# Kernel optimization log

Hardware: AMD Instinct MI355X
Metric: run time of the kernel (lower is better)

The kernel has to match this reference:

```python
import jax, jax.numpy as jnp
import numpy as np
import math

N_FILT = 80
FILT_DIM = 251
FS = 16000
MIN_FREQ = 50.0
MIN_BAND = 50.0


def _init_params():
    low_freq_mel = 80.0
    high_freq_mel = 2595.0 * np.log10(1.0 + FS / 2.0 / 700.0)
    mel_points = np.linspace(low_freq_mel, high_freq_mel, N_FILT)
    f_cos = 700.0 * (10.0 ** (mel_points / 2595.0) - 1.0)
    b1 = np.roll(f_cos, 1)
    b2 = np.roll(f_cos, -1)
    b1[0] = 30.0
    b2[-1] = FS / 2.0 - 100.0
    freq_scale = FS * 1.0
    return (jnp.asarray(b1 / freq_scale, dtype=jnp.float32),
            jnp.asarray((b2 - b1) / freq_scale, dtype=jnp.float32))


def setup_inputs() -> dict:
    key = jax.random.key(0)
    x = jax.random.normal(key, (32, 1, 32000), dtype=jnp.float32)
    filt_b1, filt_band = _init_params()
    return {"x": x, "filt_b1": filt_b1, "filt_band": filt_band}


def _sinc_batch(band, t_right):
    # band: [F] (in Hz, already scaled by fs); t_right: [T] (seconds)
    arg = 2.0 * math.pi * band[:, None] * t_right[None, :]  # [F, T]
    y_right = jnp.sin(arg) / arg
    y_left = y_right[:, ::-1]
    ones = jnp.ones((band.shape[0], 1), dtype=band.dtype)
    return jnp.concatenate([y_left, ones, y_right], axis=1)  # [F, 2T+1]


def _build_filters(filt_b1, filt_band):
    N = FILT_DIM
    freq_scale = float(FS)
    t_right = (jnp.linspace(1.0, (N - 1) / 2.0, (N - 1) // 2) / FS).astype(jnp.float32)
    filt_beg = jnp.abs(filt_b1) + MIN_FREQ / freq_scale            # [F]
    filt_end = filt_beg + (jnp.abs(filt_band) + MIN_BAND / freq_scale)
    # torch.linspace(0, N, steps=N): N points from 0 to N inclusive
    n = jnp.linspace(0.0, float(N), N).astype(jnp.float32)
    window = (0.54 - 0.46 * jnp.cos(2.0 * math.pi * n / N)).astype(jnp.float32)
    low_pass1 = 2.0 * filt_beg[:, None] * _sinc_batch(filt_beg * freq_scale, t_right)
    low_pass2 = 2.0 * filt_end[:, None] * _sinc_batch(filt_end * freq_scale, t_right)
    band_pass = low_pass2 - low_pass1                              # [F, N]
    band_pass = band_pass / jnp.max(band_pass, axis=1, keepdims=True)
    return band_pass * window[None, :]                             # [F, N]


def reference(x, filt_b1, filt_band):
    filters = _build_filters(filt_b1, filt_band)                   # [N_filt, Filt_dim]
    out = jax.lax.conv_general_dilated(
        x, filters[:, None, :],
        window_strides=(1,), padding='VALID',
        dimension_numbers=('NCH', 'OIH', 'NCH'))
    return out  # [B, N_filt, L - Filt_dim + 1]
```

## Files before the change

### kernel.cpp

```cpp
#include <hip/hip_runtime.h>
#include <math.h>

#define N_FILT   80
#define FILT_DIM 251
#define KPAD     256
#define SIG_LEN  32000
#define OUT_LEN  31750
#define BATCH    32
#define TPB      320

#define STRIP    1024
#define NREP     8
#define LROW     644
#define OBS2     36

#define TWO_PI_F 6.28318530717958647692f

typedef __attribute__((ext_vector_type(8))) short    short8;
typedef __attribute__((ext_vector_type(8))) _Float16 half8;
typedef __attribute__((ext_vector_type(4))) float    float4v;
typedef __attribute__((ext_vector_type(2))) float    float2v;

__global__ __launch_bounds__(256) void build_filters_kernel(
    const float* __restrict__ b1, const float* __restrict__ band,
    unsigned short* __restrict__ fh)
{
    const int f = blockIdx.x;
    const int i = threadIdx.x;

    const float MINF = 50.0f / 16000.0f;
    const float fb = fabsf(b1[f]) + MINF;
    const float fe = fb + fabsf(band[f]) + MINF;

    float v = 0.0f;
    if (i < FILT_DIM) {
        int m = i - 125; m = (m < 0) ? -m : m;
        if (m == 0) v = 2.0f * fe - 2.0f * fb;
        else {
            float a1 = TWO_PI_F * fb * (float)m;
            float a2 = TWO_PI_F * fe * (float)m;
            v = 2.0f * fe * (sinf(a2) / a2) - 2.0f * fb * (sinf(a1) / a1);
        }
    }

    __shared__ float red[256];
    red[i] = (i < FILT_DIM) ? v : -INFINITY;
    __syncthreads();
    #pragma unroll
    for (int s = 128; s > 0; s >>= 1) {
        if (i < s) red[i] = fmaxf(red[i], red[i + s]);
        __syncthreads();
    }
    const float mx = red[0];

    const float w   = 0.54f - 0.46f * cosf(TWO_PI_F * (float)i / 250.0f);
    const float val = (i < FILT_DIM) ? (v / mx) * w : 0.0f;
    const _Float16 h = (_Float16)val;
    fh[f * KPAD + i] = __builtin_bit_cast(unsigned short, h);
}

__global__ __launch_bounds__(TPB, 7) void sinc_mfma_kernel(
    const float* __restrict__ x,
    const unsigned short* __restrict__ fh,
    float* __restrict__ out)
{
    __shared__ __align__(16) unsigned xf[NREP * LROW];
    __shared__ __align__(16) float    ob[5][16 * OBS2];

    const int tid = threadIdx.x;
    const unsigned raw = blockIdx.x;
    const unsigned swz = (raw & 7u) * 128u + (raw >> 3);
    const int strip = (int)(swz & 31u);
    const int n     = (int)(swz >> 5);
    const int e0    = strip * STRIP;
    const float* xp = x + (size_t)n * SIG_LEN;

    for (int d = tid; d < LROW; d += TPB) {
        const int g = e0 + 2 * d;
        float v0, v1, v2;
        if (g + 2 < SIG_LEN) {
            float2 p = *(const float2*)(xp + g);
            v0 = p.x; v1 = p.y; v2 = xp[g + 2];
        } else {
            v0 = (g     < SIG_LEN) ? xp[g]     : 0.0f;
            v1 = (g + 1 < SIG_LEN) ? xp[g + 1] : 0.0f;
            v2 = (g + 2 < SIG_LEN) ? xp[g + 2] : 0.0f;
        }
        const _Float16 h0 = (_Float16)v0, h1 = (_Float16)v1, h2 = (_Float16)v2;
        union { _Float16 h[2]; unsigned u; } pe, po;
        pe.h[0] = h0; pe.h[1] = h1;
        po.h[0] = h1; po.h[1] = h2;
        xf[0 * LROW + d] = pe.u;
        xf[1 * LROW + d] = po.u;
        if (d >= 1) { xf[2 * LROW + d - 1] = pe.u;
                      xf[3 * LROW + d - 1] = po.u; }
        if (d >= 2) { xf[4 * LROW + d - 2] = pe.u;
                      xf[5 * LROW + d - 2] = po.u; }
        if (d >= 3) { xf[6 * LROW + d - 3] = pe.u;
                      xf[7 * LROW + d - 3] = po.u; }
    }

    const int lane = tid & 63;
    const int w    = tid >> 6;
    const int m    = lane & 15;
    const int q    = lane >> 4;
    short8 Ah[8];
    {
        const unsigned short* ph = fh + (w * 16 + m) * KPAD + q * 8;
        #pragma unroll
        for (int kb = 0; kb < 8; ++kb)
            Ah[kb] = *(const short8*)(ph + kb * 32);
    }
    __syncthreads();

    const int r = m & 7;
    const unsigned base = (unsigned)(r * LROW + 4 * (m >> 3) + 4 * q);

    float* const obw  = &ob[w][0];
    const int    cp   = 2 * (lane & 15);
    const int    rr0  = lane >> 4;
    const size_t row0 = ((size_t)n * N_FILT + w * 16) * OUT_LEN;

    for (int gp = 0; gp < 32; ++gp) {
        #pragma unroll
        for (int tl = 0; tl < 2; ++tl) {
            const int tt = gp * 2 + tl;
            float4v a0 = {0.f,0.f,0.f,0.f}, a1 = {0.f,0.f,0.f,0.f};
            const unsigned o0 = base + 8u * (unsigned)tt;
            #pragma unroll
            for (int kk = 0; kk < 4; ++kk) {
                a0 = __builtin_amdgcn_mfma_f32_16x16x32_f16(
                         __builtin_bit_cast(half8, Ah[2*kk]),
                         __builtin_bit_cast(half8, *(const uint4*)(&xf[o0 + 32*kk])),
                         a0, 0, 0, 0);
                a1 = __builtin_amdgcn_mfma_f32_16x16x32_f16(
                         __builtin_bit_cast(half8, Ah[2*kk+1]),
                         __builtin_bit_cast(half8, *(const uint4*)(&xf[o0 + 32*kk + 16])),
                         a1, 0, 0, 0);
            }
            const int oc = tl * 16 + m;
            #pragma unroll
            for (int rg = 0; rg < 4; ++rg)
                obw[(q * 4 + rg) * OBS2 + oc] = a0[rg] + a1[rg];
        }

        const int t0 = e0 + gp * 32 + cp;
        if (t0 + 1 < OUT_LEN) {
            #pragma unroll
            for (int j = 0; j < 4; ++j) {
                const int row = j * 4 + rr0;
                const float2v v = *(const float2v*)(&obw[row * OBS2 + cp]);
                *(float2v*)(out + row0 + (size_t)row * OUT_LEN + t0) = v;
            }
        }
    }
}

extern "C" void kernel_launch(void* const* d_in, const int* in_sizes, int n_in,
                              void* d_out, int out_size, void* d_ws, size_t ws_size,
                              hipStream_t stream)
{
    const float* x    = (const float*)d_in[0];
    const float* b1   = (const float*)d_in[1];
    const float* band = (const float*)d_in[2];
    float* outp = (float*)d_out;

    unsigned short* fh = (unsigned short*)d_ws;

    build_filters_kernel<<<dim3(N_FILT), dim3(256), 0, stream>>>(b1, band, fh);

    dim3 grid(1024);
    sinc_mfma_kernel<<<grid, dim3(TPB), 0, stream>>>(x, fh, outp);
}
```

Before: 84.79 us.

## Fuse filter construction into conv kernel and apply max normalization to outputs

```diff
diff --git a/kernel.cpp b/kernel.cpp
--- a/kernel.cpp
+++ b/kernel.cpp
@@ -3,7 +3,6 @@
 
 #define N_FILT   80
 #define FILT_DIM 251
-#define KPAD     256
 #define SIG_LEN  32000
 #define OUT_LEN  31750
 #define BATCH    32
@@ -21,47 +20,10 @@
 typedef __attribute__((ext_vector_type(4))) float    float4v;
 typedef __attribute__((ext_vector_type(2))) float    float2v;
 
-__global__ __launch_bounds__(256) void build_filters_kernel(
-    const float* __restrict__ b1, const float* __restrict__ band,
-    unsigned short* __restrict__ fh)
-{
-    const int f = blockIdx.x;
-    const int i = threadIdx.x;
-
-    const float MINF = 50.0f / 16000.0f;
-    const float fb = fabsf(b1[f]) + MINF;
-    const float fe = fb + fabsf(band[f]) + MINF;
-
-    float v = 0.0f;
-    if (i < FILT_DIM) {
-        int m = i - 125; m = (m < 0) ? -m : m;
-        if (m == 0) v = 2.0f * fe - 2.0f * fb;
-        else {
-            float a1 = TWO_PI_F * fb * (float)m;
-            float a2 = TWO_PI_F * fe * (float)m;
-            v = 2.0f * fe * (sinf(a2) / a2) - 2.0f * fb * (sinf(a1) / a1);
-        }
-    }
-
-    __shared__ float red[256];
-    red[i] = (i < FILT_DIM) ? v : -INFINITY;
-    __syncthreads();
-    #pragma unroll
-    for (int s = 128; s > 0; s >>= 1) {
-        if (i < s) red[i] = fmaxf(red[i], red[i + s]);
-        __syncthreads();
-    }
-    const float mx = red[0];
-
-    const float w   = 0.54f - 0.46f * cosf(TWO_PI_F * (float)i / 250.0f);
-    const float val = (i < FILT_DIM) ? (v / mx) * w : 0.0f;
-    const _Float16 h = (_Float16)val;
-    fh[f * KPAD + i] = __builtin_bit_cast(unsigned short, h);
-}
-
 __global__ __launch_bounds__(TPB, 7) void sinc_mfma_kernel(
     const float* __restrict__ x,
-    const unsigned short* __restrict__ fh,
+    const float* __restrict__ b1,
+    const float* __restrict__ band,
     float* __restrict__ out)
 {
     __shared__ __align__(16) unsigned xf[NREP * LROW];
@@ -104,13 +66,48 @@
     const int w    = tid >> 6;
     const int m    = lane & 15;
     const int q    = lane >> 4;
+
+    const int fg = w * 16 + m;
+    const float MINF = 50.0f / 16000.0f;
+    const float fbv = fabsf(b1[fg]) + MINF;
+    const float fev = fbv + fabsf(band[fg]) + MINF;
+    float mx = -INFINITY;
     short8 Ah[8];
-    {
-        const unsigned short* ph = fh + (w * 16 + m) * KPAD + q * 8;
+    #pragma unroll
+    for (int kb = 0; kb < 8; ++kb) {
+        union { unsigned short u[8]; short8 s; } pk;
         #pragma unroll
-        for (int kb = 0; kb < 8; ++kb)
-            Ah[kb] = *(const short8*)(ph + kb * 32);
+        for (int j = 0; j < 8; ++j) {
+            const int i = 32 * kb + 8 * q + j;
+            if (i < FILT_DIM) {
+                int mm = i - 125; mm = (mm < 0) ? -mm : mm;
+                float v;
+                if (mm == 0) v = 2.0f * fev - 2.0f * fbv;
+                else {
+                    const float a1 = TWO_PI_F * fbv * (float)mm;
+                    const float a2 = TWO_PI_F * fev * (float)mm;
+                    v = 2.0f * fev * (sinf(a2) / a2)
+                      - 2.0f * fbv * (sinf(a1) / a1);
+                }
+                mx = fmaxf(mx, v);
+                const float wdw =
+                    0.54f - 0.46f * cosf(TWO_PI_F * (float)i / 250.0f);
+                const _Float16 hv = (_Float16)(v * wdw);
+                pk.u[j] = __builtin_bit_cast(unsigned short, hv);
+            } else {
+                pk.u[j] = 0;
+            }
+        }
+        Ah[kb] = pk.s;
     }
+    mx = fmaxf(mx, __shfl_xor(mx, 16));
+    mx = fmaxf(mx, __shfl_xor(mx, 32));
+    const float rs = 1.0f / mx;
+    float rsv[4];
+    #pragma unroll
+    for (int j = 0; j < 4; ++j)
+        rsv[j] = __shfl(rs, q * 4 + j);
+
     __syncthreads();
 
     const int r = m & 7;
@@ -141,7 +138,7 @@
             const int oc = tl * 16 + m;
             #pragma unroll
             for (int rg = 0; rg < 4; ++rg)
-                obw[(q * 4 + rg) * OBS2 + oc] = a0[rg] + a1[rg];
+                obw[(q * 4 + rg) * OBS2 + oc] = (a0[rg] + a1[rg]) * rsv[rg];
         }
 
         const int t0 = e0 + gp * 32 + cp;
@@ -165,10 +162,8 @@
     const float* band = (const float*)d_in[2];
     float* outp = (float*)d_out;
 
-    unsigned short* fh = (unsigned short*)d_ws;
-
-    build_filters_kernel<<<dim3(N_FILT), dim3(256), 0, stream>>>(b1, band, fh);
+    (void)d_ws; (void)ws_size;
 
     dim3 grid(1024);
-    sinc_mfma_kernel<<<grid, dim3(TPB), 0, stream>>>(x, fh, outp);
+    sinc_mfma_kernel<<<grid, dim3(TPB), 0, stream>>>(x, b1, band, outp);
 }
```

Measured after the change: 206.2 us. 2.43x slower.
